# Optimization experiments

Measured on AMD Instinct MI355X. Metric: run time of the kernel, lower is better.

The kernel has to match this reference:

```python
import jax, jax.numpy as jnp
import numpy as np

DIM = 192
HEADS = 4
EPS_LN = 1e-5
EPS_NORM = 1e-12


def _layernorm(x, w, b):
    # x: [b, c, h, w]; normalize over channel dim (equiv to 'b (h w) c' LN over last axis)
    mu = jnp.mean(x, axis=1, keepdims=True)
    var = jnp.mean((x - mu) ** 2, axis=1, keepdims=True)
    return (x - mu) / jnp.sqrt(var + EPS_LN) * w[None, :, None, None] + b[None, :, None, None]


def _conv1x1(x, w):
    # w: [out_c, in_c]
    return jnp.einsum('bchw,oc->bohw', x, w)


def _dwconv3x3(x, w):
    # w: [c, 1, 3, 3], depthwise (groups = c), padding 1
    return jax.lax.conv_general_dilated(
        x, w, window_strides=(1, 1), padding='SAME',
        feature_group_count=x.shape[1],
        dimension_numbers=('NCHW', 'OIHW', 'NCHW'))


def _l2norm(x):
    # F.normalize(dim=-1): x / max(||x||_2, eps)
    n = jnp.sqrt(jnp.sum(x * x, axis=-1, keepdims=True))
    return x / jnp.maximum(n, EPS_NORM)


def setup_inputs() -> dict:
    key = jax.random.key(0)
    ks = jax.random.split(key, 10)
    b, c, h, w = 8, DIM, 128, 128
    inp = {
        'xx': jax.random.normal(ks[0], (b, c, h, w), jnp.float32),
        'q_in': jax.random.normal(ks[1], (b, c, h, w), jnp.float32),
        'ln_w': jnp.ones((c,), jnp.float32),
        'ln_b': jnp.zeros((c,), jnp.float32),
        'w_q': jax.random.normal(ks[2], (c, c), jnp.float32) * 0.02,
        'w_k': jax.random.normal(ks[3], (c, c), jnp.float32) * 0.02,
        'w_v': jax.random.normal(ks[4], (c, c), jnp.float32) * 0.02,
        'wd_q': jax.random.normal(ks[5], (c, 1, 3, 3), jnp.float32) * 0.1,
        'wd_k': jax.random.normal(ks[6], (c, 1, 3, 3), jnp.float32) * 0.1,
        'wd_v': jax.random.normal(ks[7], (c, 1, 3, 3), jnp.float32) * 0.1,
        'w_proj': jax.random.normal(ks[8], (c, c), jnp.float32) * 0.02,
        'temperature': jnp.ones((HEADS, 1, 1), jnp.float32),
    }
    return inp


def reference(xx, q_in, ln_w, ln_b, w_q, w_k, w_v, wd_q, wd_k, wd_v, w_proj, temperature):
    b, c, h, w = xx.shape
    hw = h * w
    dh = c // HEADS  # per-head channel dim

    x_n = _layernorm(xx, ln_w, ln_b)
    q_n = _layernorm(q_in, ln_w, ln_b)

    q = _dwconv3x3(_conv1x1(q_n, w_q), wd_q)
    k = _dwconv3x3(_conv1x1(x_n, w_k), wd_k)
    v = _dwconv3x3(_conv1x1(x_n, w_v), wd_v)

    # b (head c) h w -> b head c (h w)
    q = q.reshape(b, HEADS, dh, hw)
    k = k.reshape(b, HEADS, dh, hw)
    v = v.reshape(b, HEADS, dh, hw)

    q = _l2norm(q)
    k = _l2norm(k)

    # channel-channel attention: [b, head, dh, dh]
    attn = jnp.einsum('bhcn,bhdn->bhcd', q, k) * temperature[None]
    attn = jax.nn.softmax(attn, axis=-1)

    out = jnp.einsum('bhcd,bhdn->bhcn', attn, v)  # [b, head, dh, hw]
    out = out.reshape(b, c, h, w)
    out = _conv1x1(out, w_proj) + q_in
    return out
```

## Files before the change

kernel.cpp:

```cpp
#include <hip/hip_runtime.h>
#include <hip/hip_bf16.h>
#include <stdint.h>

#define HWSZ 16384
#define CCH 192
#define NB 8
#define NHEAD 4
#define DHEAD 48

typedef unsigned short u16;
typedef __bf16 bf16x8 __attribute__((ext_vector_type(8)));
typedef float f32x4 __attribute__((ext_vector_type(4)));
typedef short s16x8 __attribute__((ext_vector_type(8)));
typedef short s16x4 __attribute__((ext_vector_type(4)));

__device__ __forceinline__ float b2f(u16 h){
  union { unsigned u; float f; } v; v.u = ((unsigned)h) << 16; return v.f;
}
__device__ __forceinline__ u16 f2b(float f){
  union { float f; unsigned u; } v; v.f = f;
  unsigned r = v.u + 0x7fffu + ((v.u >> 16) & 1u);
  return (u16)(r >> 16);
}

__global__ __launch_bounds__(256) void k_ln_t(
    const float* __restrict__ x, const float* __restrict__ lnw,
    const float* __restrict__ lnb, u16* __restrict__ out)
{
  __shared__ float xs[CCH * 66];
  __shared__ float red[512];
  int tid = threadIdx.x;
  int bx  = blockIdx.x;
  int b    = bx >> 8;
  int tile = bx & 255;
  int p0   = tile * 64;

  float wl = 0.f, bl = 0.f;
  if (tid >= 64){
    int c = tid - 64;
    wl = lnw[c]; bl = lnb[c];
  }

  {
    const float* xb = x + (size_t)b * CCH * HWSZ + p0;
    int cq = tid >> 4;
    int q  = tid & 15;
    float4 v[12];
    #pragma unroll
    for (int i = 0; i < 12; ++i){
      int c = i * 16 + cq;
      v[i] = *(const float4*)(xb + (size_t)c * HWSZ + q * 4);
    }
    #pragma unroll
    for (int i = 0; i < 12; ++i){
      int c = i * 16 + cq;
      float* dst = &xs[c * 66 + q * 4];
      *(float2*)(dst)     = make_float2(v[i].x, v[i].y);
      *(float2*)(dst + 2) = make_float2(v[i].z, v[i].w);
    }
  }
  __syncthreads();

  {
    int w = tid >> 6, l = tid & 63;
    float s = 0.f, ss = 0.f;
    #pragma unroll
    for (int j = 0; j < 48; ++j){
      float v = xs[(48 * w + j) * 66 + l];
      s += v; ss += v * v;
    }
    red[w * 64 + l]       = s;
    red[256 + w * 64 + l] = ss;
  }
  __syncthreads();

  float mu = 0.f, rs = 0.f;
  if (tid < 64){
    float s  = red[tid]       + red[64 + tid]  + red[128 + tid] + red[192 + tid];
    float ss = red[256 + tid] + red[320 + tid] + red[384 + tid] + red[448 + tid];
    mu = s * (1.f / CCH);
    float var = ss * (1.f / CCH) - mu * mu;
    rs = rsqrtf(var + 1e-5f);
  }
  __syncthreads();
  if (tid < 64){ red[tid] = mu; red[64 + tid] = rs; }
  else { int c = tid - 64; red[128 + c] = wl; red[320 + c] = bl; }
  __syncthreads();

  {
    u16* ob = out + ((size_t)b * HWSZ + p0) * CCH;
    int px = tid >> 2;
    int cb = tid & 3;
    float m = red[px];
    float r = red[64 + px];
    #pragma unroll
    for (int i = 0; i < 6; ++i){
      int c8 = cb + i * 4;
      int c0 = c8 * 8;
      s16x8 pk;
      #pragma unroll
      for (int j = 0; j < 8; ++j){
        int c = c0 + j;
        float o = (xs[c * 66 + px] - m) * r * red[128 + c] + red[320 + c];
        pk[j] = (short)f2b(o);
      }
      *(s16x8*)(&ob[(size_t)px * CCH + c0]) = pk;
    }
  }
}

template<int F32OUT>
__global__ __launch_bounds__(256, 2) void k_gemm(
    const float* __restrict__ A, const u16* __restrict__ Bm,
    void* __restrict__ Outv, const float* __restrict__ resid)
{
  __shared__ u16 lA[64 * 200];
  __shared__ u16 lB[128 * 200];
  int tid = threadIdx.x;
  int n0 = blockIdx.x * 128;
  int m0 = blockIdx.y * 64;
  int b  = blockIdx.z;
  {
    const float* ap = A + m0 * CCH;
    #pragma unroll
    for (int i = 0; i < 6; ++i){
      int off = (i * 256 + tid) * 8;
      float4 v0 = *(const float4*)(ap + off);
      float4 v1 = *(const float4*)(ap + off + 4);
      int row = off / CCH, col = off - row * CCH;
      s16x8 pk;
      pk[0] = (short)f2b(v0.x); pk[1] = (short)f2b(v0.y);
      pk[2] = (short)f2b(v0.z); pk[3] = (short)f2b(v0.w);
      pk[4] = (short)f2b(v1.x); pk[5] = (short)f2b(v1.y);
      pk[6] = (short)f2b(v1.z); pk[7] = (short)f2b(v1.w);
      *(s16x8*)(&lA[row * 200 + col]) = pk;
    }
  }
  {
    const u16* bp = Bm + ((size_t)b * HWSZ + n0) * CCH;
    #pragma unroll
    for (int i = 0; i < 12; ++i){
      int off = (i * 256 + tid) * 8;
      int4 v = *(const int4*)(bp + off);
      int row = off / CCH, col = off - row * CCH;
      *(int4*)(&lB[row * 200 + col]) = v;
    }
  }
  __syncthreads();
  int lane = tid & 63, wid = tid >> 6;
  int quad = lane >> 4, r = lane & 15;
  int wm = (wid >> 1) * 32, wn = (wid & 1) * 64;
  f32x4 acc[2][4] = {};
  #pragma unroll
  for (int k0 = 0; k0 < CCH; k0 += 32){
    bf16x8 af[2], bfr[4];
    #pragma unroll
    for (int i = 0; i < 2; ++i)
      af[i] = *(const bf16x8*)(&lA[(wm + i * 16 + r) * 200 + k0 + quad * 8]);
    #pragma unroll
    for (int j = 0; j < 4; ++j)
      bfr[j] = *(const bf16x8*)(&lB[(wn + j * 16 + r) * 200 + k0 + quad * 8]);
    #pragma unroll
    for (int i = 0; i < 2; ++i)
      #pragma unroll
      for (int j = 0; j < 4; ++j)
        acc[i][j] = __builtin_amdgcn_mfma_f32_16x16x32_bf16(af[i], bfr[j], acc[i][j], 0, 0, 0);
  }
  size_t obase = (size_t)b * CCH * HWSZ;
  #pragma unroll
  for (int i = 0; i < 2; ++i){
    #pragma unroll
    for (int rg = 0; rg < 4; ++rg){
      int o = m0 + wm + i * 16 + quad * 4 + rg;
      size_t rowb = obase + (size_t)o * HWSZ;
      #pragma unroll
      for (int j = 0; j < 4; ++j){
        int n = n0 + wn + j * 16 + r;
        float vv = acc[i][j][rg];
        if (F32OUT){
          ((float*)Outv)[rowb + n] = vv + resid[rowb + n];
        } else {
          ((u16*)Outv)[rowb + n] = f2b(vv);
        }
      }
    }
  }
}

__global__ __launch_bounds__(256) void k_dw3(
    const float* __restrict__ wq, const float* __restrict__ wk,
    const float* __restrict__ wv,
    u16* __restrict__ bq, u16* __restrict__ bk, u16* __restrict__ bv,
    float* __restrict__ ssq_q, float* __restrict__ ssq_k)
{
  __shared__ u16 pln[HWSZ];
  int tid = threadIdx.x;
  int bc  = blockIdx.x;
  int z   = blockIdx.y;
  int c   = bc % CCH;
  const float* wd = (z == 0) ? wq : (z == 1) ? wk : wv;
  u16* buf = (z == 0) ? bq : (z == 1) ? bk : bv;
  float w[9];
  #pragma unroll
  for (int t = 0; t < 9; ++t) w[t] = wd[c * 9 + t];
  u16* p = buf + (size_t)bc * HWSZ;
  {
    int4* lp = (int4*)pln;
    const int4* gp = (const int4*)p;
    #pragma unroll
    for (int i = 0; i < 8; ++i) lp[i * 256 + tid] = gp[i * 256 + tid];
  }
  __syncthreads();
  float ss = 0.f;
  #pragma unroll
  for (int i = 0; i < 8; ++i){
    int s  = i * 256 + tid;
    int y  = s >> 4;
    int x0 = (s & 15) << 3;
    float acc[8] = {0.f,0.f,0.f,0.f,0.f,0.f,0.f,0.f};
    #pragma unroll
    for (int dy = 0; dy < 3; ++dy){
      int yy = y + dy - 1;
      if (yy < 0 || yy > 127) continue;
      int base = yy * 128 + x0;
      s16x8 cv = *(const s16x8*)(&pln[base]);
      float c8[8];
      #pragma unroll
      for (int j = 0; j < 8; ++j) c8[j] = b2f((u16)cv[j]);
      float lft = (x0 > 0)   ? b2f(pln[base - 1]) : 0.f;
      float rgt = (x0 < 120) ? b2f(pln[base + 8]) : 0.f;
      float wl = w[dy * 3], wc = w[dy * 3 + 1], wr = w[dy * 3 + 2];
      acc[0] += wl * lft + wc * c8[0] + wr * c8[1];
      #pragma unroll
      for (int j = 1; j < 7; ++j)
        acc[j] += wl * c8[j - 1] + wc * c8[j] + wr * c8[j + 1];
      acc[7] += wl * c8[6] + wc * c8[7] + wr * rgt;
    }
    s16x8 pk;
    #pragma unroll
    for (int j = 0; j < 8; ++j){
      pk[j] = (short)f2b(acc[j]);
      ss += acc[j] * acc[j];
    }
    *(s16x8*)(p + y * 128 + x0) = pk;
  }
  if (z < 2){
    #pragma unroll
    for (int m = 32; m > 0; m >>= 1) ss += __shfl_xor(ss, m);
    if ((tid & 63) == 0) atomicAdd(&((z == 0) ? ssq_q : ssq_k)[bc], ss);
  }
}

__global__ void k_gram(const u16* __restrict__ q, const u16* __restrict__ k,
                       float* __restrict__ G)
{
  int tid = threadIdx.x;
  int chunk = blockIdx.x;
  int h = blockIdx.y, b = blockIdx.z;
  int lane = tid & 63, w = tid >> 6;
  int quad = lane >> 4, r = lane & 15;
  int nb = chunk * 1024 + w * 256;
  const u16* qb = q + ((size_t)b * CCH + h * DHEAD) * HWSZ;
  const u16* kb = k + ((size_t)b * CCH + h * DHEAD) * HWSZ;
  f32x4 acc[3][3] = {};
  for (int s = 0; s < 8; ++s){
    int kk = nb + s * 32 + quad * 8;
    bf16x8 af[3], bfr[3];
    #pragma unroll
    for (int i = 0; i < 3; ++i){
      af[i]  = *(const bf16x8*)(qb + (size_t)(i * 16 + r) * HWSZ + kk);
      bfr[i] = *(const bf16x8*)(kb + (size_t)(i * 16 + r) * HWSZ + kk);
    }
    #pragma unroll
    for (int i = 0; i < 3; ++i)
      #pragma unroll
      for (int j = 0; j < 3; ++j)
        acc[i][j] = __builtin_amdgcn_mfma_f32_16x16x32_bf16(af[i], bfr[j], acc[i][j], 0, 0, 0);
  }
  float* gb = G + (size_t)(b * NHEAD + h) * (DHEAD * DHEAD);
  #pragma unroll
  for (int i = 0; i < 3; ++i)
    #pragma unroll
    for (int j = 0; j < 3; ++j)
      #pragma unroll
      for (int rg = 0; rg < 4; ++rg){
        int row = i * 16 + quad * 4 + rg;
        int col = j * 16 + r;
        atomicAdd(&gb[row * DHEAD + col], acc[i][j][rg]);
      }
}

__global__ __launch_bounds__(256) void k_mk(
    const float* __restrict__ G, const float* __restrict__ ssq_q,
    const float* __restrict__ ssq_k, const float* __restrict__ temp,
    const float* __restrict__ wp, u16* __restrict__ Mout)
{
  __shared__ u16 Pt[48 * 72];
  __shared__ u16 wA[192 * 72];
  __shared__ float rks[48];
  int tid = threadIdx.x;
  int h = blockIdx.x, b = blockIdx.y;
  {
    s16x8 z = {};
    #pragma unroll
    for (int i = 0; i < 2; ++i){
      int idx = (i * 256 + tid) * 8;
      if (idx < 48 * 72) *(s16x8*)(&Pt[idx]) = z;
    }
    #pragma unroll
    for (int i = 0; i < 7; ++i){
      int idx = (i * 256 + tid) * 8;
      if (idx < 192 * 72) *(s16x8*)(&wA[idx]) = z;
    }
  }
  if (tid < DHEAD)
    rks[tid] = 1.f / fmaxf(sqrtf(ssq_k[b * CCH + h * DHEAD + tid]), 1e-12f);
  __syncthreads();
  if (tid < DHEAD){
    float rq = temp[h] / fmaxf(sqrtf(ssq_q[b * CCH + h * DHEAD + tid]), 1e-12f);
    const float* gr = G + (size_t)(b * NHEAD + h) * (DHEAD * DHEAD) + tid * DHEAD;
    float a[DHEAD];
    float mx = -1e30f;
    #pragma unroll
    for (int d = 0; d < DHEAD; ++d){
      a[d] = gr[d] * rq * rks[d];
      mx = fmaxf(mx, a[d]);
    }
    float sum = 0.f;
    #pragma unroll
    for (int d = 0; d < DHEAD; ++d){ a[d] = __expf(a[d] - mx); sum += a[d]; }
    float inv = 1.f / sum;
    #pragma unroll
    for (int d = 0; d < DHEAD; ++d) Pt[d * 72 + tid] = f2b(a[d] * inv);
  }
  {
    const float* wb = wp + h * DHEAD;
    #pragma unroll
    for (int i = 0; i < 9; ++i){
      int e = (i * 256 + tid) * 4;
      int row = e / DHEAD, col = e - row * DHEAD;
      float4 v = *(const float4*)(wb + (size_t)row * CCH + col);
      s16x4 pk;
      pk[0] = (short)f2b(v.x); pk[1] = (short)f2b(v.y);
      pk[2] = (short)f2b(v.z); pk[3] = (short)f2b(v.w);
      *(s16x4*)(&wA[row * 72 + col]) = pk;
    }
  }
  __syncthreads();
  int lane = tid & 63, wid = tid >> 6;
  int quad = lane >> 4, r = lane & 15;
  int wm = wid * 48;
  f32x4 acc[3][3] = {};
  #pragma unroll
  for (int ks = 0; ks < 2; ++ks){
    int k0 = ks * 32;
    bf16x8 af[3], bf[3];
    #pragma unroll
    for (int i = 0; i < 3; ++i)
      af[i] = *(const bf16x8*)(&wA[(wm + i * 16 + r) * 72 + k0 + quad * 8]);
    #pragma unroll
    for (int j = 0; j < 3; ++j)
      bf[j] = *(const bf16x8*)(&Pt[(j * 16 + r) * 72 + k0 + quad * 8]);
    #pragma unroll
    for (int i = 0; i < 3; ++i)
      #pragma unroll
      for (int j = 0; j < 3; ++j)
        acc[i][j] = __builtin_amdgcn_mfma_f32_16x16x32_bf16(af[i], bf[j], acc[i][j], 0, 0, 0);
  }
  u16* mb = Mout + (size_t)b * (CCH * CCH) + h * DHEAD;
  #pragma unroll
  for (int i = 0; i < 3; ++i)
    #pragma unroll
    for (int j = 0; j < 3; ++j)
      #pragma unroll
      for (int rg = 0; rg < 4; ++rg){
        int o = wm + i * 16 + quad * 4 + rg;
        int d = j * 16 + r;
        mb[(size_t)o * CCH + d] = f2b(acc[i][j][rg]);
      }
}

__global__ __launch_bounds__(256) void k_gemmv(
    const u16* __restrict__ M, const u16* __restrict__ V,
    float* __restrict__ Out, const float* __restrict__ resid)
{
  __shared__ u16 lA[64 * 200];
  __shared__ u16 lV[96 * 264];
  int tid = threadIdx.x;
  int n0 = blockIdx.x * 128;
  int m0 = blockIdx.y * 64;
  int b  = blockIdx.z;
  {
    const u16* ap = M + (size_t)b * (CCH * CCH) + m0 * CCH;
    #pragma unroll
    for (int i = 0; i < 6; ++i){
      int off = (i * 256 + tid) * 8;
      int row = off / CCH, col = off - row * CCH;
      *(int4*)(&lA[row * 200 + col]) = *(const int4*)(ap + off);
    }
  }
  {
    const u16* vp = V + (size_t)b * CCH * HWSZ + n0;
    #pragma unroll
    for (int i = 0; i < 12; ++i){
      int e = i * 256 + tid;
      int c = e >> 4, ns = (e & 15) * 8;
      int4 v = *(const int4*)(vp + (size_t)c * HWSZ + ns);
      int kb = c >> 5, kr = c & 31;
      int tile = (kr >> 2) & 1;
      int mr = ((kr >> 3) << 2) | (kr & 3);
      int ti = (kb * 8 + (ns >> 4)) * 2 + tile;
      *(int4*)(&lV[ti * 264 + mr * 16 + (ns & 15)]) = v;
    }
  }
  __syncthreads();
  int lane = tid & 63, wid = tid >> 6;
  int quad = lane >> 4, r = lane & 15;
  int wm = (wid >> 1) * 32, wn = (wid & 1) * 64;
  unsigned lvb = (unsigned)(uintptr_t)(&lV[0]) + 2u * (unsigned)(r + quad * 64)
               + (unsigned)((wn >> 4) * 2) * 528u;
  f32x4 acc[2][4] = {};
  #pragma unroll
  for (int kb = 0; kb < 6; ++kb){
    int k0 = kb * 32;
    s16x4 lo[4], hi[4];
    #pragma unroll
    for (int j = 0; j < 4; ++j){
      unsigned a = lvb + (unsigned)kb * 8448u + (unsigned)j * 1056u;
      asm volatile("ds_read_b64_tr_b16 %0, %1" : "=&v"(lo[j]) : "v"(a));
      asm volatile("ds_read_b64_tr_b16 %0, %1 offset:528" : "=&v"(hi[j]) : "v"(a));
    }
    bf16x8 af[2];
    #pragma unroll
    for (int i = 0; i < 2; ++i)
      af[i] = *(const bf16x8*)(&lA[(wm + i * 16 + r) * 200 + k0 + quad * 8]);
    asm volatile("s_waitcnt lgkmcnt(0)" ::: "memory");
    __builtin_amdgcn_sched_barrier(0);
    #pragma unroll
    for (int j = 0; j < 4; ++j){
      union { s16x8 s; bf16x8 b; } u;
      u.s = __builtin_shufflevector(lo[j], hi[j], 0, 1, 2, 3, 4, 5, 6, 7);
      #pragma unroll
      for (int i = 0; i < 2; ++i)
        acc[i][j] = __builtin_amdgcn_mfma_f32_16x16x32_bf16(af[i], u.b, acc[i][j], 0, 0, 0);
    }
  }
  size_t obase = (size_t)b * CCH * HWSZ;
  #pragma unroll
  for (int i = 0; i < 2; ++i){
    #pragma unroll
    for (int rg = 0; rg < 4; ++rg){
      int o = m0 + wm + i * 16 + quad * 4 + rg;
      size_t rowb = obase + (size_t)o * HWSZ;
      #pragma unroll
      for (int j = 0; j < 4; ++j){
        int n = n0 + wn + j * 16 + r;
        Out[rowb + n] = acc[i][j][rg] + resid[rowb + n];
      }
    }
  }
}

extern "C" void kernel_launch(void* const* d_in, const int* in_sizes, int n_in,
                              void* d_out, int out_size, void* d_ws, size_t ws_size,
                              hipStream_t stream)
{
  const float* xx     = (const float*)d_in[0];
  const float* q_in   = (const float*)d_in[1];
  const float* ln_w   = (const float*)d_in[2];
  const float* ln_b   = (const float*)d_in[3];
  const float* w_q    = (const float*)d_in[4];
  const float* w_k    = (const float*)d_in[5];
  const float* w_v    = (const float*)d_in[6];
  const float* wd_q   = (const float*)d_in[7];
  const float* wd_k   = (const float*)d_in[8];
  const float* wd_v   = (const float*)d_in[9];
  const float* w_proj = (const float*)d_in[10];
  const float* temp   = (const float*)d_in[11];

  const size_t SZ = (size_t)NB * CCH * HWSZ;
  u16* B1 = (u16*)d_ws;
  u16* B2 = B1 + SZ;
  u16* B3 = B2 + SZ;
  float* G     = (float*)(B3 + SZ);
  float* ssq_q = G + 32 * DHEAD * DHEAD;
  float* ssq_k = ssq_q + NB * CCH;
  u16* Mb      = (u16*)(ssq_k + NB * CCH);
  u16* lnbuf   = (u16*)d_out;

  hipMemsetAsync(G, 0, (size_t)(32 * DHEAD * DHEAD + 2 * NB * CCH) * sizeof(float), stream);

  dim3 gg(128, 3, NB);
  k_ln_t<<<NB * 256, 256, 0, stream>>>(xx, ln_w, ln_b, lnbuf);
  k_gemm<0><<<gg, 256, 0, stream>>>(w_k, lnbuf, B2, nullptr);
  k_gemm<0><<<gg, 256, 0, stream>>>(w_v, lnbuf, B1, nullptr);
  k_ln_t<<<NB * 256, 256, 0, stream>>>(q_in, ln_w, ln_b, lnbuf);
  k_gemm<0><<<gg, 256, 0, stream>>>(w_q, lnbuf, B3, nullptr);
  k_dw3<<<dim3(NB * CCH, 3), 256, 0, stream>>>(wd_q, wd_k, wd_v,
                                               B3, B2, B1, ssq_q, ssq_k);
  k_gram<<<dim3(16, NHEAD, NB), 256, 0, stream>>>(B3, B2, G);
  k_mk<<<dim3(NHEAD, NB), 256, 0, stream>>>(G, ssq_q, ssq_k, temp, w_proj, Mb);
  k_gemmv<<<gg, 256, 0, stream>>>(Mb, B1, (float*)d_out, q_in);
}
```

Baseline: 478.0 us.

## Fuse LayerNorm into QKV 1x1 GEMMs and stream depthwise conv via registers

```diff
diff --git a/kernel.cpp b/kernel.cpp
--- a/kernel.cpp
+++ b/kernel.cpp
@@ -23,17 +23,38 @@
   return (u16)(r >> 16);
 }
 
-__global__ __launch_bounds__(256) void k_ln_t(
+__global__ __launch_bounds__(256) void k_wpack(
+    const float* __restrict__ wq, const float* __restrict__ wk,
+    const float* __restrict__ wv, u16* __restrict__ o)
+{
+  int m = blockIdx.x;
+  const float* src = (m == 0) ? wq : (m == 1) ? wk : wv;
+  u16* dst = o + (size_t)m * CCH * CCH;
+  int tid = threadIdx.x;
+  #pragma unroll
+  for (int i = 0; i < 36; ++i){
+    int e = (i * 256 + tid) * 4;
+    float4 v = *(const float4*)(src + e);
+    s16x4 pk;
+    pk[0] = (short)f2b(v.x); pk[1] = (short)f2b(v.y);
+    pk[2] = (short)f2b(v.z); pk[3] = (short)f2b(v.w);
+    *(s16x4*)(dst + e) = pk;
+  }
+}
+
+template<int NG>
+__global__ __launch_bounds__(256) void k_lngemm(
     const float* __restrict__ x, const float* __restrict__ lnw,
-    const float* __restrict__ lnb, u16* __restrict__ out)
+    const float* __restrict__ lnb,
+    const u16* __restrict__ W0, const u16* __restrict__ W1,
+    u16* __restrict__ O0, u16* __restrict__ O1)
 {
   __shared__ float xs[CCH * 66];
   __shared__ float red[512];
+  __shared__ u16 lnX[64 * 200];
   int tid = threadIdx.x;
-  int bx  = blockIdx.x;
-  int b    = bx >> 8;
-  int tile = bx & 255;
-  int p0   = tile * 64;
+  int b   = blockIdx.y;
+  int p0  = blockIdx.x * 64;
 
   float wl = 0.f, bl = 0.f;
   if (tid >= 64){
@@ -88,15 +109,13 @@
   __syncthreads();
 
   {
-    u16* ob = out + ((size_t)b * HWSZ + p0) * CCH;
     int px = tid >> 2;
     int cb = tid & 3;
     float m = red[px];
     float r = red[64 + px];
     #pragma unroll
     for (int i = 0; i < 6; ++i){
-      int c8 = cb + i * 4;
-      int c0 = c8 * 8;
+      int c0 = (cb + i * 4) * 8;
       s16x8 pk;
       #pragma unroll
       for (int j = 0; j < 8; ++j){
@@ -104,84 +123,59 @@
         float o = (xs[c * 66 + px] - m) * r * red[128 + c] + red[320 + c];
         pk[j] = (short)f2b(o);
       }
-      *(s16x8*)(&ob[(size_t)px * CCH + c0]) = pk;
-    }
-  }
-}
-
-template<int F32OUT>
-__global__ __launch_bounds__(256, 2) void k_gemm(
-    const float* __restrict__ A, const u16* __restrict__ Bm,
-    void* __restrict__ Outv, const float* __restrict__ resid)
-{
-  __shared__ u16 lA[64 * 200];
-  __shared__ u16 lB[128 * 200];
-  int tid = threadIdx.x;
-  int n0 = blockIdx.x * 128;
-  int m0 = blockIdx.y * 64;
-  int b  = blockIdx.z;
-  {
-    const float* ap = A + m0 * CCH;
-    #pragma unroll
-    for (int i = 0; i < 6; ++i){
-      int off = (i * 256 + tid) * 8;
-      float4 v0 = *(const float4*)(ap + off);
-      float4 v1 = *(const float4*)(ap + off + 4);
-      int row = off / CCH, col = off - row * CCH;
-      s16x8 pk;
-      pk[0] = (short)f2b(v0.x); pk[1] = (short)f2b(v0.y);
-      pk[2] = (short)f2b(v0.z); pk[3] = (short)f2b(v0.w);
-      pk[4] = (short)f2b(v1.x); pk[5] = (short)f2b(v1.y);
-      pk[6] = (short)f2b(v1.z); pk[7] = (short)f2b(v1.w);
-      *(s16x8*)(&lA[row * 200 + col]) = pk;
-    }
-  }
-  {
-    const u16* bp = Bm + ((size_t)b * HWSZ + n0) * CCH;
-    #pragma unroll
-    for (int i = 0; i < 12; ++i){
-      int off = (i * 256 + tid) * 8;
-      int4 v = *(const int4*)(bp + off);
-      int row = off / CCH, col = off - row * CCH;
-      *(int4*)(&lB[row * 200 + col]) = v;
-    }
-  }
-  __syncthreads();
+      *(s16x8*)(&lnX[px * 200 + c0]) = pk;
+    }
+  }
+  __syncthreads();
+
   int lane = tid & 63, wid = tid >> 6;
   int quad = lane >> 4, r = lane & 15;
-  int wm = (wid >> 1) * 32, wn = (wid & 1) * 64;
-  f32x4 acc[2][4] = {};
-  #pragma unroll
-  for (int k0 = 0; k0 < CCH; k0 += 32){
-    bf16x8 af[2], bfr[4];
-    #pragma unroll
-    for (int i = 0; i < 2; ++i)
-      af[i] = *(const bf16x8*)(&lA[(wm + i * 16 + r) * 200 + k0 + quad * 8]);
+  int wm = wid * 48;
+  const u16* A0 = W0 + (size_t)wm * CCH;
+  const u16* A1 = (NG == 2) ? (W1 + (size_t)wm * CCH) : nullptr;
+  f32x4 acc0[3][4] = {};
+  f32x4 acc1[3][4] = {};
+  #pragma unroll
+  for (int ks = 0; ks < 6; ++ks){
+    int k0 = ks * 32;
+    bf16x8 bfv[4];
     #pragma unroll
     for (int j = 0; j < 4; ++j)
-      bfr[j] = *(const bf16x8*)(&lB[(wn + j * 16 + r) * 200 + k0 + quad * 8]);
-    #pragma unroll
-    for (int i = 0; i < 2; ++i)
+      bfv[j] = *(const bf16x8*)(&lnX[(j * 16 + r) * 200 + k0 + quad * 8]);
+    bf16x8 a0[3], a1[3];
+    #pragma unroll
+    for (int i = 0; i < 3; ++i)
+      a0[i] = *(const bf16x8*)(A0 + (size_t)(i * 16 + r) * CCH + k0 + quad * 8);
+    if (NG == 2){
+      #pragma unroll
+      for (int i = 0; i < 3; ++i)
+        a1[i] = *(const bf16x8*)(A1 + (size_t)(i * 16 + r) * CCH + k0 + quad * 8);
+    }
+    #pragma unroll
+    for (int i = 0; i < 3; ++i)
       #pragma unroll
       for (int j = 0; j < 4; ++j)
-        acc[i][j] = __builtin_amdgcn_mfma_f32_16x16x32_bf16(af[i], bfr[j], acc[i][j], 0, 0, 0);
-  }
-  size_t obase = (size_t)b * CCH * HWSZ;
-  #pragma unroll
-  for (int i = 0; i < 2; ++i){
+        acc0[i][j] = __builtin_amdgcn_mfma_f32_16x16x32_bf16(a0[i], bfv[j], acc0[i][j], 0, 0, 0);
+    if (NG == 2){
+      #pragma unroll
+      for (int i = 0; i < 3; ++i)
+        #pragma unroll
+        for (int j = 0; j < 4; ++j)
+          acc1[i][j] = __builtin_amdgcn_mfma_f32_16x16x32_bf16(a1[i], bfv[j], acc1[i][j], 0, 0, 0);
+    }
+  }
+  size_t ob = (size_t)b * CCH * HWSZ;
+  #pragma unroll
+  for (int i = 0; i < 3; ++i){
     #pragma unroll
     for (int rg = 0; rg < 4; ++rg){
-      int o = m0 + wm + i * 16 + quad * 4 + rg;
-      size_t rowb = obase + (size_t)o * HWSZ;
+      int o = wm + i * 16 + quad * 4 + rg;
+      size_t rowb = ob + (size_t)o * HWSZ;
       #pragma unroll
       for (int j = 0; j < 4; ++j){
-        int n = n0 + wn + j * 16 + r;
-        float vv = acc[i][j][rg];
-        if (F32OUT){
-          ((float*)Outv)[rowb + n] = vv + resid[rowb + n];
-        } else {
-          ((u16*)Outv)[rowb + n] = f2b(vv);
-        }
+        int n = p0 + j * 16 + r;
+        O0[rowb + n] = f2b(acc0[i][j][rg]);
+        if (NG == 2) O1[rowb + n] = f2b(acc1[i][j][rg]);
       }
     }
   }
@@ -193,7 +187,6 @@
     u16* __restrict__ bq, u16* __restrict__ bk, u16* __restrict__ bv,
     float* __restrict__ ssq_q, float* __restrict__ ssq_k)
 {
-  __shared__ u16 pln[HWSZ];
   int tid = threadIdx.x;
   int bc  = blockIdx.x;
   int z   = blockIdx.y;
@@ -204,37 +197,44 @@
   #pragma unroll
   for (int t = 0; t < 9; ++t) w[t] = wd[c * 9 + t];
   u16* p = buf + (size_t)bc * HWSZ;
-  {
-    int4* lp = (int4*)pln;
-    const int4* gp = (const int4*)p;
-    #pragma unroll
-    for (int i = 0; i < 8; ++i) lp[i * 256 + tid] = gp[i * 256 + tid];
-  }
-  __syncthreads();
+
+  int xseg = tid & 15, ygrp = tid >> 4;
+  int x0 = xseg * 8, y0 = ygrp * 8;
+
+  s16x8 zz = {0,0,0,0,0,0,0,0};
+  s16x8 raw[10];
+  #pragma unroll
+  for (int rr = 0; rr < 10; ++rr){
+    int yy = y0 - 1 + rr;
+    raw[rr] = (yy >= 0 && yy < 128) ? *(const s16x8*)(p + yy * 128 + x0) : zz;
+  }
+  __syncthreads();
+
+  float cf[10][8];
+  float lf[10], rgt[10];
+  #pragma unroll
+  for (int rr = 0; rr < 10; ++rr){
+    #pragma unroll
+    for (int j = 0; j < 8; ++j) cf[rr][j] = b2f((u16)raw[rr][j]);
+    float l  = __shfl_up(cf[rr][7], 1);
+    float rr_ = __shfl_down(cf[rr][0], 1);
+    lf[rr]  = (xseg > 0)  ? l   : 0.f;
+    rgt[rr] = (xseg < 15) ? rr_ : 0.f;
+  }
+
   float ss = 0.f;
   #pragma unroll
-  for (int i = 0; i < 8; ++i){
-    int s  = i * 256 + tid;
-    int y  = s >> 4;
-    int x0 = (s & 15) << 3;
+  for (int k = 0; k < 8; ++k){
     float acc[8] = {0.f,0.f,0.f,0.f,0.f,0.f,0.f,0.f};
     #pragma unroll
     for (int dy = 0; dy < 3; ++dy){
-      int yy = y + dy - 1;
-      if (yy < 0 || yy > 127) continue;
-      int base = yy * 128 + x0;
-      s16x8 cv = *(const s16x8*)(&pln[base]);
-      float c8[8];
-      #pragma unroll
-      for (int j = 0; j < 8; ++j) c8[j] = b2f((u16)cv[j]);
-      float lft = (x0 > 0)   ? b2f(pln[base - 1]) : 0.f;
-      float rgt = (x0 < 120) ? b2f(pln[base + 8]) : 0.f;
+      int rr = k + dy;
       float wl = w[dy * 3], wc = w[dy * 3 + 1], wr = w[dy * 3 + 2];
-      acc[0] += wl * lft + wc * c8[0] + wr * c8[1];
+      acc[0] += wl * lf[rr] + wc * cf[rr][0] + wr * cf[rr][1];
       #pragma unroll
       for (int j = 1; j < 7; ++j)
-        acc[j] += wl * c8[j - 1] + wc * c8[j] + wr * c8[j + 1];
-      acc[7] += wl * c8[6] + wc * c8[7] + wr * rgt;
+        acc[j] += wl * cf[rr][j - 1] + wc * cf[rr][j] + wr * cf[rr][j + 1];
+      acc[7] += wl * cf[rr][6] + wc * cf[rr][7] + wr * rgt[rr];
     }
     s16x8 pk;
     #pragma unroll
@@ -242,8 +242,9 @@
       pk[j] = (short)f2b(acc[j]);
       ss += acc[j] * acc[j];
     }
-    *(s16x8*)(p + y * 128 + x0) = pk;
-  }
+    *(s16x8*)(p + (y0 + k) * 128 + x0) = pk;
+  }
+
   if (z < 2){
     #pragma unroll
     for (int m = 32; m > 0; m >>= 1) ss += __shfl_xor(ss, m);
@@ -254,6 +255,7 @@
 __global__ void k_gram(const u16* __restrict__ q, const u16* __restrict__ k,
                        float* __restrict__ G)
 {
+  __shared__ float gs[4 * 48 * 49];
   int tid = threadIdx.x;
   int chunk = blockIdx.x;
   int h = blockIdx.y, b = blockIdx.z;
@@ -277,7 +279,7 @@
       for (int j = 0; j < 3; ++j)
         acc[i][j] = __builtin_amdgcn_mfma_f32_16x16x32_bf16(af[i], bfr[j], acc[i][j], 0, 0, 0);
   }
-  float* gb = G + (size_t)(b * NHEAD + h) * (DHEAD * DHEAD);
+  float* gw = gs + w * (48 * 49);
   #pragma unroll
   for (int i = 0; i < 3; ++i)
     #pragma unroll
@@ -286,8 +288,18 @@
       for (int rg = 0; rg < 4; ++rg){
         int row = i * 16 + quad * 4 + rg;
         int col = j * 16 + r;
-        atomicAdd(&gb[row * DHEAD + col], acc[i][j][rg]);
+        gw[row * 49 + col] = acc[i][j][rg];
       }
+  __syncthreads();
+  float* gb = G + (size_t)(b * NHEAD + h) * (DHEAD * DHEAD);
+  #pragma unroll
+  for (int t = 0; t < 9; ++t){
+    int e = t * 256 + tid;
+    int row = e / 48, col = e - row * 48;
+    int o = row * 49 + col;
+    float s = gs[o] + gs[48 * 49 + o] + gs[2 * 48 * 49 + o] + gs[3 * 48 * 49 + o];
+    atomicAdd(&gb[e], s);
+  }
 }
 
 __global__ __launch_bounds__(256) void k_mk(
@@ -486,19 +498,18 @@
   float* ssq_q = G + 32 * DHEAD * DHEAD;
   float* ssq_k = ssq_q + NB * CCH;
   u16* Mb      = (u16*)(ssq_k + NB * CCH);
-  u16* lnbuf   = (u16*)d_out;
+  u16* Wb      = Mb + (size_t)NB * CCH * CCH;
 
   hipMemsetAsync(G, 0, (size_t)(32 * DHEAD * DHEAD + 2 * NB * CCH) * sizeof(float), stream);
 
-  dim3 gg(128, 3, NB);
-  k_ln_t<<<NB * 256, 256, 0, stream>>>(xx, ln_w, ln_b, lnbuf);
-  k_gemm<0><<<gg, 256, 0, stream>>>(w_k, lnbuf, B2, nullptr);
-  k_gemm<0><<<gg, 256, 0, stream>>>(w_v, lnbuf, B1, nullptr);
-  k_ln_t<<<NB * 256, 256, 0, stream>>>(q_in, ln_w, ln_b, lnbuf);
-  k_gemm<0><<<gg, 256, 0, stream>>>(w_q, lnbuf, B3, nullptr);
+  k_wpack<<<3, 256, 0, stream>>>(w_q, w_k, w_v, Wb);
+  k_lngemm<2><<<dim3(256, NB), 256, 0, stream>>>(
+      xx, ln_w, ln_b, Wb + CCH * CCH, Wb + 2 * CCH * CCH, B2, B1);
+  k_lngemm<1><<<dim3(256, NB), 256, 0, stream>>>(
+      q_in, ln_w, ln_b, Wb, nullptr, B3, nullptr);
   k_dw3<<<dim3(NB * CCH, 3), 256, 0, stream>>>(wd_q, wd_k, wd_v,
                                                B3, B2, B1, ssq_q, ssq_k);
   k_gram<<<dim3(16, NHEAD, NB), 256, 0, stream>>>(B3, B2, G);
   k_mk<<<dim3(NHEAD, NB), 256, 0, stream>>>(G, ssq_q, ssq_k, temp, w_proj, Mb);
-  k_gemmv<<<gg, 256, 0, stream>>>(Mb, B1, (float*)d_out, q_in);
-}
+  k_gemmv<<<dim3(128, 3, NB), 256, 0, stream>>>(Mb, B1, (float*)d_out, q_in);
+}
```

Measured after the change: 433.5 us. -9.3%, faster.
